# Optimization experiments

Measured on AMD Instinct MI355X. Metric: run time of the kernel, lower is better.

The kernel has to match this reference:

```python
import jax, jax.numpy as jnp
import numpy as np

B, S, D = 1, 2048, 2048
H, KV = 32, 8
HD = D // H          # 64
R = H // KV          # 4 (GQA repeat factor)
ROPE_BASE = 10000.0


def setup_inputs() -> dict:
    key = jax.random.key(0)
    ks = jax.random.split(key, 5)
    x = jax.random.normal(ks[0], (B, S, D), jnp.float32)
    # Real rotary frequencies as (cos, sin) pairs: [S, HD//2, 2]
    inv_freq = 1.0 / (ROPE_BASE ** (np.arange(0, HD, 2, dtype=np.float64) / HD))
    ang = np.outer(np.arange(S, dtype=np.float64), inv_freq)
    freqs_cis = jnp.asarray(np.stack([np.cos(ang), np.sin(ang)], axis=-1), jnp.float32)
    std = 0.02
    wq = jax.random.normal(ks[1], (H * HD, D), jnp.float32) * std
    wk = jax.random.normal(ks[2], (KV * HD, D), jnp.float32) * std
    wv = jax.random.normal(ks[3], (KV * HD, D), jnp.float32) * std
    wo = jax.random.normal(ks[4], (D, H * HD), jnp.float32) * std
    return {"x": x, "freqs_cis": freqs_cis, "wq": wq, "wk": wk, "wv": wv, "wo": wo}


def _apply_rope(x, cos, sin):
    # x: [b, s, h, hd]; cos/sin: [s, hd//2]. Complex multiply on interleaved pairs.
    xr = x.reshape(*x.shape[:-1], HD // 2, 2)
    x0, x1 = xr[..., 0], xr[..., 1]
    c = cos[None, :, None, :]
    s = sin[None, :, None, :]
    o0 = x0 * c - x1 * s
    o1 = x0 * s + x1 * c
    return jnp.stack([o0, o1], axis=-1).reshape(x.shape)


def reference(x, freqs_cis, wq, wk, wv, wo):
    b, s, _ = x.shape
    q = (x @ wq.T).reshape(b, s, H, HD)
    k = (x @ wk.T).reshape(b, s, KV, HD)
    v = (x @ wv.T).reshape(b, s, KV, HD)
    cos, sin = freqs_cis[..., 0], freqs_cis[..., 1]
    q = _apply_rope(q, cos, sin)
    k = _apply_rope(k, cos, sin)
    # GQA: group q heads instead of repeat_interleave on k/v.
    # repeat_interleave maps kv-head g -> q heads [g*R, (g+1)*R), matching this reshape.
    qg = q.reshape(b, s, KV, R, HD)
    scale = 1.0 / np.sqrt(HD)
    scores = jnp.einsum('bsgrd,btgd->bgrst', qg, k) * scale  # [b, KV, R, s, t]
    causal = jnp.tril(jnp.ones((s, s), dtype=bool))
    scores = jnp.where(causal, scores, jnp.float32(-1e9))
    attn = jax.nn.softmax(scores.astype(jnp.float32), axis=-1).astype(q.dtype)
    out = jnp.einsum('bgrst,btgd->bsgrd', attn, v).reshape(b, s, H * HD)
    return out @ wo.T
```

## Files before the change

kernel.cpp:

```cpp
#include <hip/hip_runtime.h>

typedef unsigned short u16;
typedef unsigned int u32;
typedef __bf16 bf16x8 __attribute__((ext_vector_type(8)));
typedef unsigned short ushort8 __attribute__((ext_vector_type(8)));
typedef float floatx4 __attribute__((ext_vector_type(4)));
typedef u32 u32x2 __attribute__((ext_vector_type(2)));

#define S_LEN 2048
#define NH 32
#define NKV 8
#define HD_ 64
#define LDQ 3072

__device__ __forceinline__ u16 f2bf(float f) {
  unsigned u = __builtin_bit_cast(unsigned, f);
  u += 0x7FFF + ((u >> 16) & 1);
  return (u16)(u >> 16);
}
__device__ __forceinline__ float bf2f(u16 h) {
  unsigned u = ((unsigned)h) << 16;
  return __builtin_bit_cast(float, u);
}
__device__ __forceinline__ bf16x8 ld8(const u16* p) {
  return __builtin_bit_cast(bf16x8, *(const ushort8*)p);
}
__device__ __forceinline__ floatx4 mfma16(bf16x8 a, bf16x8 b, floatx4 c) {
  return __builtin_amdgcn_mfma_f32_16x16x32_bf16(a, b, c, 0, 0, 0);
}
__device__ __forceinline__ u32 pk2bf(float a, float b) {
  u32 ua = __builtin_bit_cast(u32, a) + 0x8000u;
  u32 ub = __builtin_bit_cast(u32, b) + 0x8000u;
  return __builtin_amdgcn_perm(ub, ua, 0x07060302);
}

__global__ void cvt_kernel(const float* __restrict__ in, u16* __restrict__ out, int n4) {
  int i = blockIdx.x * blockDim.x + threadIdx.x;
  if (i >= n4) return;
  float4 v = ((const float4*)in)[i];
  ((ushort4*)out)[i] = make_ushort4(f2bf(v.x), f2bf(v.y), f2bf(v.z), f2bf(v.w));
}

template <int TM, int TN, int OUT_BF16>
__global__ __launch_bounds__(256) void gemm_db(
    const u16* __restrict__ A, const u16* __restrict__ B, void* __restrict__ C,
    int ldc, int K, int lda) {
  __shared__ __align__(16) u16 As[2][TM * 64];
  __shared__ __align__(16) u16 Bs[2][TN * 64];
  const int tid = threadIdx.x;
  const int wave = tid >> 6, lane = tid & 63;
  const int quad = lane >> 4, l16 = lane & 15;
  const int nwg = gridDim.x * gridDim.y;
  int lin = (int)blockIdx.y * gridDim.x + blockIdx.x;
  lin = (lin & 7) * (nwg >> 3) + (lin >> 3);
  const int bm = (lin % gridDim.y) * TM, bn = (lin / gridDim.y) * TN;
  const int wr = (wave >> 1) * (TM / 2), wc = (wave & 1) * (TN / 2);
  constexpr int MI = TM / 32, NI = TN / 32;
  const int crow = tid >> 3, col8 = tid & 7;

  size_t aoff[MI], boff[NI];
#pragma unroll
  for (int j = 0; j < MI; j++) aoff[j] = (size_t)(bm + crow + j * 32) * lda + col8 * 8;
#pragma unroll
  for (int j = 0; j < NI; j++) boff[j] = (size_t)(bn + crow + j * 32) * K + col8 * 8;

  ushort8 a8[MI], b8[NI];
  auto load_tiles = [&](int k0) {
#pragma unroll
    for (int j = 0; j < MI; j++) a8[j] = *(const ushort8*)(A + aoff[j] + k0);
#pragma unroll
    for (int j = 0; j < NI; j++) b8[j] = *(const ushort8*)(B + boff[j] + k0);
  };
  auto write_tiles = [&](int p) {
#pragma unroll
    for (int j = 0; j < MI; j++) {
      const int row = crow + j * 32;
      *(ushort8*)&As[p][row * 64 + ((col8 ^ (row & 7)) * 8)] = a8[j];
    }
#pragma unroll
    for (int j = 0; j < NI; j++) {
      const int row = crow + j * 32;
      *(ushort8*)&Bs[p][row * 64 + ((col8 ^ (row & 7)) * 8)] = b8[j];
    }
  };

  floatx4 acc[MI][NI] = {};
  load_tiles(0);
  write_tiles(0);
  __syncthreads();
  int p = 0;
  for (int k0 = 0; k0 < K; k0 += 64) {
    const bool more = (k0 + 64 < K);
    if (more) load_tiles(k0 + 64);
#pragma unroll
    for (int kh = 0; kh < 2; kh++) {
      bf16x8 af[MI], bfr[NI];
#pragma unroll
      for (int mi = 0; mi < MI; mi++) {
        const int row = wr + mi * 16 + l16;
        af[mi] = ld8(&As[p][row * 64 + (((kh * 4 + quad) ^ (row & 7)) * 8)]);
      }
#pragma unroll
      for (int ni = 0; ni < NI; ni++) {
        const int row = wc + ni * 16 + l16;
        bfr[ni] = ld8(&Bs[p][row * 64 + (((kh * 4 + quad) ^ (row & 7)) * 8)]);
      }
#pragma unroll
      for (int mi = 0; mi < MI; mi++)
#pragma unroll
        for (int ni = 0; ni < NI; ni++)
          acc[mi][ni] = mfma16(af[mi], bfr[ni], acc[mi][ni]);
    }
    if (more) {
      write_tiles(p ^ 1);
      __syncthreads();
      p ^= 1;
    }
  }

#pragma unroll
  for (int mi = 0; mi < MI; mi++)
#pragma unroll
    for (int ni = 0; ni < NI; ni++)
#pragma unroll
      for (int r = 0; r < 4; r++) {
        const int row = bm + wr + mi * 16 + quad * 4 + r;
        const int col = bn + wc + ni * 16 + l16;
        if (OUT_BF16) ((u16*)C)[(size_t)row * ldc + col] = f2bf(acc[mi][ni][r]);
        else          ((float*)C)[(size_t)row * ldc + col] = acc[mi][ni][r];
      }
}

__global__ void rope_kernel(u16* __restrict__ qk, const float* __restrict__ fc, int h_bits,
                            int row_stride, float scale) {
  int idx = blockIdx.x * blockDim.x + threadIdx.x;
  int d = idx & 31;
  int t = idx >> 5;
  int hh = t & ((1 << h_bits) - 1);
  int s = t >> h_bits;
  float c  = fc[s * 64 + d * 2];
  float sn = fc[s * 64 + d * 2 + 1];
  size_t base = (size_t)s * row_stride + hh * 64 + d * 2;
  float x0 = bf2f(qk[base]), x1 = bf2f(qk[base + 1]);
  qk[base]     = f2bf((x0 * c - x1 * sn) * scale);
  qk[base + 1] = f2bf((x0 * sn + x1 * c) * scale);
}

__global__ void transpose_v(const u16* __restrict__ qkv, u16* __restrict__ vT) {
  int idx = blockIdx.x * blockDim.x + threadIdx.x;
  int s = idx & (S_LEN - 1);
  int t = idx >> 11;
  vT[idx] = qkv[(size_t)s * LDQ + 2560 + t];
}

__global__ __launch_bounds__(256) void attn_kernel(const u16* qkv, const u16* __restrict__ vT,
                                                   u16* __restrict__ o) {
  __shared__ __align__(16) u16 Ks[2][64 * 64];
  __shared__ __align__(16) u16 Vs[2][64 * 64];
  __shared__ __align__(16) u16 pS[4][16 * 64];
  const int h = blockIdx.x;
  const int g = h >> 2;
  const int tid = threadIdx.x;
  const int wave = tid >> 6, lane = tid & 63;
  const int quad = lane >> 4, l16 = lane & 15;
  const int p_ = (int)blockIdx.y;
  const int qtB = 31 - p_;

  const ushort8 ones_u = {0x3F80, 0x3F80, 0x3F80, 0x3F80, 0x3F80, 0x3F80, 0x3F80, 0x3F80};
  const bf16x8 onesA = __builtin_bit_cast(bf16x8, ones_u);

  const int qrow = wave * 16 + l16;
  const int qgA = p_ * 64 + qrow, qgB = qtB * 64 + qrow;
  const size_t qoffA = (size_t)qgA * LDQ + h * HD_;
  const size_t qoffB = (size_t)qgB * LDQ + h * HD_;
  bf16x8 qfA0 = ld8(qkv + qoffA + quad * 8);
  bf16x8 qfA1 = ld8(qkv + qoffA + 32 + quad * 8);
  bf16x8 qfB0 = ld8(qkv + qoffB + quad * 8);
  bf16x8 qfB1 = ld8(qkv + qoffB + 32 + quad * 8);

  const int rs0 = tid >> 3, rs1 = rs0 + 32;
  const int col8 = tid & 7;
  const int so = (col8 ^ (rs0 & 7)) * 8;
  const int o0 = col8 * 8;
  const int x0 = (quad ^ (l16 & 7)) * 8;
  const int x1 = ((4 + quad) ^ (l16 & 7)) * 8;
  const u16* ksrc = qkv + 2048 + g * HD_;
  const u16* vsrc = vT + (size_t)g * HD_ * S_LEN;

  ushort8 kp0, kp1, vp0, vp1;
  auto gload = [&](int t) {
    const int tb = t * 64;
    kp0 = *(const ushort8*)(ksrc + (size_t)(tb + rs0) * LDQ + o0);
    kp1 = *(const ushort8*)(ksrc + (size_t)(tb + rs1) * LDQ + o0);
    vp0 = *(const ushort8*)(vsrc + (size_t)rs0 * S_LEN + tb + o0);
    vp1 = *(const ushort8*)(vsrc + (size_t)rs1 * S_LEN + tb + o0);
  };
  auto tile_of = [&](int i) { return (i <= p_) ? i : (i - p_ - 1); };

  u16* myP = &pS[wave][0];
  int pp = 0;

  gload(0);
  *(ushort8*)&Ks[0][rs0 * 64 + so] = kp0;
  *(ushort8*)&Ks[0][rs1 * 64 + so] = kp1;
  *(ushort8*)&Vs[0][rs0 * 64 + so] = vp0;
  *(ushort8*)&Vs[0][rs1 * 64 + so] = vp1;
  gload(tile_of(1));
  __syncthreads();

  auto phase = [&](int qt, int qg, bf16x8 q0, bf16x8 q1, int ibase) {
    floatx4 O[4] = {};
    floatx4 lac = {};
    for (int kt = 0; kt <= qt; kt++) {
      const int i = ibase + kt;
      const u16* Kc = &Ks[pp][0];
      const u16* Vc = &Vs[pp][0];

      bf16x8 kf[4][2];
#pragma unroll
      for (int sub = 0; sub < 4; sub++) {
        const u16* kb = Kc + (sub * 16 + l16) * 64;
        kf[sub][0] = ld8(kb + x0);
        kf[sub][1] = ld8(kb + x1);
      }
      if (i < 32) {
        *(ushort8*)&Ks[pp ^ 1][rs0 * 64 + so] = kp0;
        *(ushort8*)&Ks[pp ^ 1][rs1 * 64 + so] = kp1;
        *(ushort8*)&Vs[pp ^ 1][rs0 * 64 + so] = vp0;
        *(ushort8*)&Vs[pp ^ 1][rs1 * 64 + so] = vp1;
        if (i < 31) gload(tile_of(i + 2));
      }
      floatx4 sf[4];
#pragma unroll
      for (int sub = 0; sub < 4; sub++) {
        floatx4 s = {};
        s = mfma16(kf[sub][0], q0, s);
        s = mfma16(kf[sub][1], q1, s);
        sf[sub] = s;
      }
      if (kt == qt) {
#pragma unroll
        for (int sub = 0; sub < 4; sub++)
#pragma unroll
          for (int r = 0; r < 4; r++)
            if (kt * 64 + sub * 16 + quad * 4 + r > qg) sf[sub][r] = -INFINITY;
      }
      u32x2 pk[4];
#pragma unroll
      for (int sub = 0; sub < 4; sub++) {
        pk[sub].x = pk2bf(__builtin_amdgcn_exp2f(sf[sub][0]), __builtin_amdgcn_exp2f(sf[sub][1]));
        pk[sub].y = pk2bf(__builtin_amdgcn_exp2f(sf[sub][2]), __builtin_amdgcn_exp2f(sf[sub][3]));
      }
      bf16x8 vf[4][2];
#pragma unroll
      for (int nt = 0; nt < 4; nt++) {
        const u16* vb = Vc + (nt * 16 + l16) * 64;
        vf[nt][0] = ld8(vb + x0);
        vf[nt][1] = ld8(vb + x1);
      }
#pragma unroll
      for (int sub = 0; sub < 4; sub++) {
        const int slot = (2 * sub + (quad >> 1)) ^ (l16 & 7);
        *(u32x2*)&myP[l16 * 64 + slot * 8 + (quad & 1) * 4] = pk[sub];
      }
      asm volatile("s_waitcnt lgkmcnt(0)" ::: "memory");
      bf16x8 pf0 = ld8(&myP[l16 * 64 + x0]);
      bf16x8 pf1 = ld8(&myP[l16 * 64 + x1]);
#pragma unroll
      for (int nt = 0; nt < 4; nt++) {
        O[nt] = mfma16(vf[nt][0], pf0, O[nt]);
        O[nt] = mfma16(vf[nt][1], pf1, O[nt]);
      }
      lac = mfma16(onesA, pf0, lac);
      lac = mfma16(onesA, pf1, lac);

      if (i < 32) {
        asm volatile("s_waitcnt lgkmcnt(0)" ::: "memory");
        __builtin_amdgcn_s_barrier();
        pp ^= 1;
      }
    }
    const float inv = 1.0f / lac[0];
    const size_t ooff = (size_t)qg * 2048 + h * HD_;
#pragma unroll
    for (int nt = 0; nt < 4; nt++)
#pragma unroll
      for (int r = 0; r < 4; r++)
        o[ooff + nt * 16 + quad * 4 + r] = f2bf(O[nt][r] * inv);
  };

  phase(p_, qgA, qfA0, qfA1, 0);
  phase(qtB, qgB, qfB0, qfB1, p_ + 1);
}

extern "C" void kernel_launch(void* const* d_in, const int* in_sizes, int n_in,
                              void* d_out, int out_size, void* d_ws, size_t ws_size,
                              hipStream_t stream) {
  const float* x  = (const float*)d_in[0];
  const float* fc = (const float*)d_in[1];
  const float* wq = (const float*)d_in[2];
  const float* wk = (const float*)d_in[3];
  const float* wv = (const float*)d_in[4];
  const float* wo = (const float*)d_in[5];
  float* out = (float*)d_out;

  char* ws = (char*)d_ws;
  const size_t MB = 1024 * 1024;
  u16* qkv = (u16*)(ws);
  u16* wb  = (u16*)(ws + 12 * MB);
  u16* vTb = (u16*)(ws + 12 * MB);
  u16* wob = (u16*)(ws + 14 * MB);
  u16* ob  = (u16*)(ws + 22 * MB);
  u16* xb  = (u16*)d_out;
  (void)ws_size; (void)n_in; (void)in_sizes; (void)out_size;

  cvt_kernel<<<4096, 256, 0, stream>>>(x,  xb, 1048576);
  cvt_kernel<<<4096, 256, 0, stream>>>(wq, wb, 1048576);
  cvt_kernel<<<1024, 256, 0, stream>>>(wk, wb + (size_t)2048 * 2048, 262144);
  cvt_kernel<<<1024, 256, 0, stream>>>(wv, wb + (size_t)2560 * 2048, 262144);
  gemm_db<128, 96, 1><<<dim3(32, 16), 256, 0, stream>>>(xb, wb, qkv, LDQ, 2048, 2048);
  cvt_kernel<<<4096, 256, 0, stream>>>(wo, wob, 1048576);
  rope_kernel<<<8192, 256, 0, stream>>>(qkv, fc, 5, LDQ, 0.18033688f);
  rope_kernel<<<2048, 256, 0, stream>>>(qkv + 2048, fc, 3, LDQ, 1.0f);
  transpose_v<<<4096, 256, 0, stream>>>(qkv, vTb);
  attn_kernel<<<dim3(NH, 16), 256, 0, stream>>>(qkv, vTb, ob);
  gemm_db<128, 64, 0><<<dim3(32, 16), 256, 0, stream>>>(ob, wob, out, 2048, 2048, 2048);
}
```

Baseline: 227.1 us.

## Fuse fp32-to-bf16 conversion of inputs and weights into GEMM tile loads

Drops the five separate conversion kernels for x, wq, wk, wv and wo. The GEMMs now read fp32 directly and convert to bf16 with round-to-nearest-even when writing tiles to shared memory. The Q/K/V weights are selected per row from three separate pointers, so the concatenated weight buffer is no longer needed. This saves launches and the extra bf16 write and read pass, but each GEMM tile load now fetches twice the bytes from global memory and re-converts the same weights many times across blocks.

```diff
diff --git a/kernel.cpp b/kernel.cpp
--- a/kernel.cpp
+++ b/kernel.cpp
@@ -6,6 +6,7 @@
 typedef unsigned short ushort8 __attribute__((ext_vector_type(8)));
 typedef float floatx4 __attribute__((ext_vector_type(4)));
 typedef u32 u32x2 __attribute__((ext_vector_type(2)));
+typedef u32 u32x4 __attribute__((ext_vector_type(4)));
 
 #define S_LEN 2048
 #define NH 32
@@ -33,18 +34,22 @@
   u32 ub = __builtin_bit_cast(u32, b) + 0x8000u;
   return __builtin_amdgcn_perm(ub, ua, 0x07060302);
 }
-
-__global__ void cvt_kernel(const float* __restrict__ in, u16* __restrict__ out, int n4) {
-  int i = blockIdx.x * blockDim.x + threadIdx.x;
-  if (i >= n4) return;
-  float4 v = ((const float4*)in)[i];
-  ((ushort4*)out)[i] = make_ushort4(f2bf(v.x), f2bf(v.y), f2bf(v.z), f2bf(v.w));
-}
-
-template <int TM, int TN, int OUT_BF16>
+__device__ __forceinline__ u32 pk2bf_rne(float a, float b) {
+  u32 ua = __builtin_bit_cast(u32, a); ua += 0x7FFF + ((ua >> 16) & 1);
+  u32 ub = __builtin_bit_cast(u32, b); ub += 0x7FFF + ((ub >> 16) & 1);
+  return __builtin_amdgcn_perm(ub, ua, 0x07060302);
+}
+__device__ __forceinline__ ushort8 cvt8(float4 lo, float4 hi) {
+  u32x4 w = {pk2bf_rne(lo.x, lo.y), pk2bf_rne(lo.z, lo.w),
+             pk2bf_rne(hi.x, hi.y), pk2bf_rne(hi.z, hi.w)};
+  return __builtin_bit_cast(ushort8, w);
+}
+
+template <int TM, int TN, int OUT_BF16, int A_F32>
 __global__ __launch_bounds__(256) void gemm_db(
-    const u16* __restrict__ A, const u16* __restrict__ B, void* __restrict__ C,
-    int ldc, int K, int lda) {
+    const void* __restrict__ Av, const float* __restrict__ B0,
+    const float* __restrict__ B1, const float* __restrict__ B2,
+    int nb1, int nb2, void* __restrict__ C, int ldc, int K, int lda) {
   __shared__ __align__(16) u16 As[2][TM * 64];
   __shared__ __align__(16) u16 Bs[2][TN * 64];
   const int tid = threadIdx.x;
@@ -58,29 +63,51 @@
   constexpr int MI = TM / 32, NI = TN / 32;
   const int crow = tid >> 3, col8 = tid & 7;
 
-  size_t aoff[MI], boff[NI];
-#pragma unroll
-  for (int j = 0; j < MI; j++) aoff[j] = (size_t)(bm + crow + j * 32) * lda + col8 * 8;
-#pragma unroll
-  for (int j = 0; j < NI; j++) boff[j] = (size_t)(bn + crow + j * 32) * K + col8 * 8;
-
-  ushort8 a8[MI], b8[NI];
+  const float* aF[MI]; const u16* aH[MI]; const float* bF[NI];
+#pragma unroll
+  for (int j = 0; j < MI; j++) {
+    const int row = bm + crow + j * 32;
+    if (A_F32) aF[j] = (const float*)Av + (size_t)row * lda + col8 * 8;
+    else       aH[j] = (const u16*)Av + (size_t)row * lda + col8 * 8;
+  }
+#pragma unroll
+  for (int j = 0; j < NI; j++) {
+    const int row = bn + crow + j * 32;
+    bF[j] = (row < nb1 ? B0 + (size_t)row * K
+           : row < nb2 ? B1 + (size_t)(row - nb1) * K
+                       : B2 + (size_t)(row - nb2) * K) + col8 * 8;
+  }
+
+  float4 a4[MI][2]; ushort8 a8[MI]; float4 b4[NI][2];
   auto load_tiles = [&](int k0) {
 #pragma unroll
-    for (int j = 0; j < MI; j++) a8[j] = *(const ushort8*)(A + aoff[j] + k0);
-#pragma unroll
-    for (int j = 0; j < NI; j++) b8[j] = *(const ushort8*)(B + boff[j] + k0);
+    for (int j = 0; j < MI; j++) {
+      if (A_F32) {
+        a4[j][0] = *(const float4*)(aF[j] + k0);
+        a4[j][1] = *(const float4*)(aF[j] + k0 + 4);
+      } else {
+        a8[j] = *(const ushort8*)(aH[j] + k0);
+      }
+    }
+#pragma unroll
+    for (int j = 0; j < NI; j++) {
+      b4[j][0] = *(const float4*)(bF[j] + k0);
+      b4[j][1] = *(const float4*)(bF[j] + k0 + 4);
+    }
   };
   auto write_tiles = [&](int p) {
 #pragma unroll
     for (int j = 0; j < MI; j++) {
       const int row = crow + j * 32;
-      *(ushort8*)&As[p][row * 64 + ((col8 ^ (row & 7)) * 8)] = a8[j];
+      ushort8 w;
+      if (A_F32) w = cvt8(a4[j][0], a4[j][1]);
+      else       w = a8[j];
+      *(ushort8*)&As[p][row * 64 + ((col8 ^ (row & 7)) * 8)] = w;
     }
 #pragma unroll
     for (int j = 0; j < NI; j++) {
       const int row = crow + j * 32;
-      *(ushort8*)&Bs[p][row * 64 + ((col8 ^ (row & 7)) * 8)] = b8[j];
+      *(ushort8*)&Bs[p][row * 64 + ((col8 ^ (row & 7)) * 8)] = cvt8(b4[j][0], b4[j][1]);
     }
   };
 
@@ -307,22 +334,16 @@
   char* ws = (char*)d_ws;
   const size_t MB = 1024 * 1024;
   u16* qkv = (u16*)(ws);
-  u16* wb  = (u16*)(ws + 12 * MB);
   u16* vTb = (u16*)(ws + 12 * MB);
-  u16* wob = (u16*)(ws + 14 * MB);
   u16* ob  = (u16*)(ws + 22 * MB);
-  u16* xb  = (u16*)d_out;
   (void)ws_size; (void)n_in; (void)in_sizes; (void)out_size;
 
-  cvt_kernel<<<4096, 256, 0, stream>>>(x,  xb, 1048576);
-  cvt_kernel<<<4096, 256, 0, stream>>>(wq, wb, 1048576);
-  cvt_kernel<<<1024, 256, 0, stream>>>(wk, wb + (size_t)2048 * 2048, 262144);
-  cvt_kernel<<<1024, 256, 0, stream>>>(wv, wb + (size_t)2560 * 2048, 262144);
-  gemm_db<128, 96, 1><<<dim3(32, 16), 256, 0, stream>>>(xb, wb, qkv, LDQ, 2048, 2048);
-  cvt_kernel<<<4096, 256, 0, stream>>>(wo, wob, 1048576);
+  gemm_db<128, 96, 1, 1><<<dim3(32, 16), 256, 0, stream>>>(
+      x, wq, wk, wv, 2048, 2560, qkv, LDQ, 2048, 2048);
   rope_kernel<<<8192, 256, 0, stream>>>(qkv, fc, 5, LDQ, 0.18033688f);
   rope_kernel<<<2048, 256, 0, stream>>>(qkv + 2048, fc, 3, LDQ, 1.0f);
   transpose_v<<<4096, 256, 0, stream>>>(qkv, vTb);
   attn_kernel<<<dim3(NH, 16), 256, 0, stream>>>(qkv, vTb, ob);
-  gemm_db<128, 64, 0><<<dim3(32, 16), 256, 0, stream>>>(ob, wob, out, 2048, 2048, 2048);
-}
+  gemm_db<128, 64, 0, 0><<<dim3(32, 16), 256, 0, stream>>>(
+      ob, wo, wo, wo, 1 << 30, 1 << 30, out, 2048, 2048, 2048);
+}
```

Result: slower. 235.6 us (+3.8%).
